# Kernel tuning notes

Hardware: AMD Instinct MI355X
Metric: run time of the kernel (lower is better)

The kernel has to match this reference:

```python
import jax, jax.numpy as jnp
import numpy as np

N_NODES = 50000
N_EDGES = 600000
N_SUB = 20000
E_SUB = 120000
D = 128

def setup_inputs() -> dict:
    key = jax.random.key(0)
    ks = jax.random.split(key, 16)
    s = 1.0 / np.sqrt(D)
    inp = {
        "x": jax.random.normal(ks[0], (N_NODES, D), dtype=jnp.float32),
        "Wm": jax.random.normal(ks[1], (D, D), dtype=jnp.float32) * s,
        "bm": jnp.zeros((D,), dtype=jnp.float32),
        "Wn2s0": jax.random.normal(ks[2], (D, D), dtype=jnp.float32) * s,
        "bn2s0": jnp.zeros((D,), dtype=jnp.float32),
        "Ws2n0": jax.random.normal(ks[3], (D, D), dtype=jnp.float32) * s,
        "bs2n0": jnp.zeros((D,), dtype=jnp.float32),
        "Wn2s1": jax.random.normal(ks[4], (D, D), dtype=jnp.float32) * s,
        "bn2s1": jnp.zeros((D,), dtype=jnp.float32),
        "Ws2n1": jax.random.normal(ks[5], (D, D), dtype=jnp.float32) * s,
        "bs2n1": jnp.zeros((D,), dtype=jnp.float32),
        "neighbor_edge_index": jax.random.randint(ks[6], (2, N_EDGES), 0, N_NODES, dtype=jnp.int64),
        "sub_row0": jax.random.randint(ks[7], (E_SUB,), 0, N_NODES, dtype=jnp.int64),
        "sub_col0": jax.random.randint(ks[8], (E_SUB,), 0, N_SUB, dtype=jnp.int64),
        "sub_row1": jax.random.randint(ks[9], (E_SUB,), 0, N_NODES, dtype=jnp.int64),
        "sub_col1": jax.random.randint(ks[10], (E_SUB,), 0, N_SUB, dtype=jnp.int64),
    }
    return inp


def _level(x, row, col, Wn2s, bn2s, Ws2n, bs2n):
    # node -> substructure: gather node feats, sum-reduce into substructures
    sub_x = jax.ops.segment_sum(x[row], col, num_segments=N_SUB)  # [n_sub, D]
    sub_x = sub_x @ Wn2s + bn2s
    # substructure -> node: gather substructure feats, sum-reduce back to nodes
    msg = jax.ops.segment_sum(sub_x[col], row, num_segments=N_NODES)  # [N, D]
    msg = msg @ Ws2n + bs2n
    return x + msg


def reference(x, Wm, bm, Wn2s0, bn2s0, Ws2n0, bs2n0, Wn2s1, bn2s1, Ws2n1, bs2n1,
              neighbor_edge_index, sub_row0, sub_col0, sub_row1, sub_col1):
    src, dst = neighbor_edge_index[0], neighbor_edge_index[1]
    # message_neighbor: GIN-like sum aggregation + Linear + ReLU
    agg = jax.ops.segment_sum(x[src], dst, num_segments=N_NODES)
    x = jax.nn.relu((x + agg) @ Wm + bm)
    # substructure levels (gather -> scatter-sum -> Linear -> gather -> scatter-sum -> Linear -> residual)
    x = _level(x, sub_row0, sub_col0, Wn2s0, bn2s0, Ws2n0, bs2n0)
    x = _level(x, sub_row1, sub_col1, Wn2s1, bn2s1, Ws2n1, bs2n1)
    return x
```

## Files before the change

kernel.cpp:

```cpp
#include <hip/hip_runtime.h>

#define D 128
#define NN 50000
#define NS 20000
#define NNP 50048
#define NSP 20032
#define L_TOT (3 * NN + 2 * NS)
#define SCAN_CHUNK 1024
#define SCAN_NBLK ((L_TOT + SCAN_CHUNK - 1) / SCAN_CHUNK)
#define LDA 136

typedef short s16x8 __attribute__((ext_vector_type(8)));
typedef float f32x4 __attribute__((ext_vector_type(4)));

__device__ __forceinline__ float b2f(unsigned int u) {
    u <<= 16;
    float f; __builtin_memcpy(&f, &u, 4);
    return f;
}
__device__ __forceinline__ unsigned short f2b(float f) {
    unsigned int u; __builtin_memcpy(&u, &f, 4);
    u += 0x7fffu + ((u >> 16) & 1u);
    return (unsigned short)(u >> 16);
}
__device__ __forceinline__ void acc8(float* a, uint4 v) {
    a[0] += b2f(v.x & 0xffffu); a[1] += b2f(v.x >> 16);
    a[2] += b2f(v.y & 0xffffu); a[3] += b2f(v.y >> 16);
    a[4] += b2f(v.z & 0xffffu); a[5] += b2f(v.z >> 16);
    a[6] += b2f(v.w & 0xffffu); a[7] += b2f(v.w >> 16);
}

struct PrepArgs {
    const float* x; unsigned short* xb;
    const float* w[5]; unsigned short* wt[5];
    int* counts;
};
#define NX4 (NN * D / 4)
#define NW  (5 * 16384)
#define NC4 (L_TOT / 4)
__global__ __launch_bounds__(256) void prep_k(PrepArgs p)
{
    int i = blockIdx.x * 256 + threadIdx.x;
    if (i < NX4) {
        float4 v = ((const float4*)p.x)[i];
        ushort4 o;
        o.x = f2b(v.x); o.y = f2b(v.y); o.z = f2b(v.z); o.w = f2b(v.w);
        ((ushort4*)p.xb)[i] = o;
        return;
    }
    i -= NX4;
    if (i < NW) {
        int wi = i >> 14;
        int r  = i & 16383;
        int k = r >> 7, n = r & 127;
        p.wt[wi][n * 128 + k] = f2b(p.w[wi][k * 128 + n]);
        return;
    }
    i -= NW;
    if (i < NC4) {
        int4 z = {0, 0, 0, 0};
        ((int4*)p.counts)[i] = z;
    }
}

__global__ __launch_bounds__(256) void hist5_k(
    const int* __restrict__ s0, const int* __restrict__ s1,
    const int* __restrict__ s2, const int* __restrict__ s3,
    const int* __restrict__ s4, int* __restrict__ counts,
    int* __restrict__ rank, int nE, int eS)
{
    int e = blockIdx.x * 256 + threadIdx.x;
    int seg, base;
    if (e < nE) { seg = s0[e]; base = 0; }
    else {
        int r = e - nE;
        if      (r <     eS) { seg = s1[r];          base = NN; }
        else if (r < 2 * eS) { seg = s2[r - eS];     base = NN + NS; }
        else if (r < 3 * eS) { seg = s3[r - 2 * eS]; base = 2 * NN + NS; }
        else if (r < 4 * eS) { seg = s4[r - 3 * eS]; base = 2 * NN + 2 * NS; }
        else return;
    }
    rank[e] = atomicAdd(&counts[base + seg], 1);
}

__global__ __launch_bounds__(256) void reduce_k(const int* __restrict__ counts,
                                                int* __restrict__ blockSums, int n)
{
    __shared__ int lds[4];
    int tid = threadIdx.x;
    int base = blockIdx.x * SCAN_CHUNK;
    int s = 0;
    #pragma unroll
    for (int i = 0; i < 4; ++i) {
        int idx = base + tid + i * 256;
        if (idx < n) s += counts[idx];
    }
    #pragma unroll
    for (int off = 32; off > 0; off >>= 1) s += __shfl_down(s, off, 64);
    if ((tid & 63) == 0) lds[tid >> 6] = s;
    __syncthreads();
    if (tid == 0) blockSums[blockIdx.x] = lds[0] + lds[1] + lds[2] + lds[3];
}

__global__ __launch_bounds__(256) void scan_sums_k(int* __restrict__ blockSums, int nb)
{
    __shared__ int lds[256];
    int tid = threadIdx.x;
    lds[tid] = (tid < nb) ? blockSums[tid] : 0;
    __syncthreads();
    for (int off = 1; off < 256; off <<= 1) {
        int t = (tid >= off) ? lds[tid - off] : 0;
        __syncthreads();
        lds[tid] += t;
        __syncthreads();
    }
    if (tid < nb) blockSums[tid] = (tid > 0) ? lds[tid - 1] : 0;
}

__global__ __launch_bounds__(256) void scan_write_k(
    const int* __restrict__ counts, const int* __restrict__ blockSums,
    int* __restrict__ offsets, int n)
{
    __shared__ int lds[256];
    int tid = threadIdx.x;
    int base = blockIdx.x * SCAN_CHUNK + tid * 4;
    int v[4]; int s = 0;
    #pragma unroll
    for (int i = 0; i < 4; ++i) {
        int idx = base + i;
        int c = (idx < n) ? counts[idx] : 0;
        v[i] = c; s += c;
    }
    lds[tid] = s;
    __syncthreads();
    for (int off = 1; off < 256; off <<= 1) {
        int t = (tid >= off) ? lds[tid - off] : 0;
        __syncthreads();
        lds[tid] += t;
        __syncthreads();
    }
    int run = blockSums[blockIdx.x] + (tid > 0 ? lds[tid - 1] : 0);
    #pragma unroll
    for (int i = 0; i < 4; ++i) {
        int idx = base + i;
        run += v[i];
        if (idx < n) offsets[idx + 1] = run;
    }
    if (blockIdx.x == 0 && tid == 0) offsets[0] = 0;
}

__global__ __launch_bounds__(256) void fill5_k(
    const int* __restrict__ s0, const int* __restrict__ v0,
    const int* __restrict__ s1, const int* __restrict__ v1,
    const int* __restrict__ s2, const int* __restrict__ v2,
    const int* __restrict__ s3, const int* __restrict__ v3,
    const int* __restrict__ s4, const int* __restrict__ v4,
    const int* __restrict__ offsets, const int* __restrict__ rank,
    int* __restrict__ perm, int nE, int eS)
{
    int e = blockIdx.x * 256 + threadIdx.x;
    int seg, val, base;
    if (e < nE) { seg = s0[e]; val = v0[e]; base = 0; }
    else {
        int r = e - nE;
        if      (r <     eS) { seg = s1[r];          val = v1[r];          base = NN; }
        else if (r < 2 * eS) { seg = s2[r - eS];     val = v2[r - eS];     base = NN + NS; }
        else if (r < 3 * eS) { seg = s3[r - 2 * eS]; val = v3[r - 2 * eS]; base = 2 * NN + NS; }
        else if (r < 4 * eS) { seg = s4[r - 3 * eS]; val = v4[r - 3 * eS]; base = 2 * NN + 2 * NS; }
        else return;
    }
    perm[offsets[base + seg] + rank[e]] = val;
}

__global__ __launch_bounds__(256, 6) void gg_k(
    const unsigned short* __restrict__ feat, const int* __restrict__ offsets,
    const int* __restrict__ perm, const unsigned short* __restrict__ addend,
    const unsigned short* __restrict__ Wt, const float* __restrict__ bias,
    const unsigned short* __restrict__ Rb, const float* __restrict__ Rf,
    float* __restrict__ outF, unsigned short* __restrict__ outB,
    int M, int relu)
{
    __shared__ unsigned short a_lds[64 * LDA];

    const int tid = threadIdx.x;
    const int r0  = blockIdx.x * 64;

    const uint4* f4 = (const uint4*)feat;
    const int lane16 = tid & 15;
    #pragma unroll
    for (int p = 0; p < 4; ++p) {
        int rloc = p * 16 + (tid >> 4);
        int s = r0 + rloc;
        float a[8] = {0.f, 0.f, 0.f, 0.f, 0.f, 0.f, 0.f, 0.f};
        if (s < M) {
            float b[8] = {0.f, 0.f, 0.f, 0.f, 0.f, 0.f, 0.f, 0.f};
            if (addend) {
                uint4 v = ((const uint4*)(addend + (size_t)s * D))[lane16];
                acc8(a, v);
            }
            int beg = offsets[s], end = offsets[s + 1];
            int j = beg;
            for (; j + 3 < end; j += 4) {
                int e0 = perm[j], e1 = perm[j + 1], e2 = perm[j + 2], e3 = perm[j + 3];
                uint4 v0 = f4[(size_t)e0 * 16 + lane16];
                uint4 v1 = f4[(size_t)e1 * 16 + lane16];
                uint4 v2 = f4[(size_t)e2 * 16 + lane16];
                uint4 v3 = f4[(size_t)e3 * 16 + lane16];
                acc8(a, v0); acc8(b, v1); acc8(a, v2); acc8(b, v3);
            }
            for (; j < end; ++j)
                acc8(a, f4[(size_t)perm[j] * 16 + lane16]);
            #pragma unroll
            for (int i = 0; i < 8; ++i) a[i] += b[i];
        }
        uint4 o;
        o.x = (unsigned int)f2b(a[0]) | ((unsigned int)f2b(a[1]) << 16);
        o.y = (unsigned int)f2b(a[2]) | ((unsigned int)f2b(a[3]) << 16);
        o.z = (unsigned int)f2b(a[4]) | ((unsigned int)f2b(a[5]) << 16);
        o.w = (unsigned int)f2b(a[6]) | ((unsigned int)f2b(a[7]) << 16);
        *((uint4*)&a_lds[rloc * LDA + lane16 * 8]) = o;
    }
    __syncthreads();

    const int lane = tid & 63;
    const int w    = tid >> 6;
    const int ln   = lane & 15;
    const int quad = lane >> 4;

    s16x8 af[4];
    const unsigned short* arow = &a_lds[(w * 16 + ln) * LDA + quad * 8];
    #pragma unroll
    for (int kc = 0; kc < 4; ++kc)
        af[kc] = *((const s16x8*)(arow + kc * 32));

    const int rbase = r0 + w * 16 + quad * 4;
    const s16x8* wt8 = (const s16x8*)Wt;

    #pragma unroll
    for (int nt = 0; nt < 8; ++nt) {
        f32x4 acc = {0.f, 0.f, 0.f, 0.f};
        const s16x8* brow = wt8 + (nt * 16 + ln) * 16 + quad;
        #pragma unroll
        for (int kc = 0; kc < 4; ++kc) {
            s16x8 bf = brow[kc * 4];
            acc = __builtin_amdgcn_mfma_f32_16x16x32_bf16(af[kc], bf, acc, 0, 0, 0);
        }
        int col = nt * 16 + ln;
        float bc = bias[col];
        #pragma unroll
        for (int r = 0; r < 4; ++r) {
            int row = rbase + r;
            if (row < M) {
                float v = acc[r] + bc;
                size_t gi = (size_t)row * D + col;
                if (Rf) v += Rf[gi];
                if (Rb) v += b2f((unsigned int)Rb[gi]);
                if (relu) v = fmaxf(v, 0.f);
                if (outF) outF[gi] = v;
                if (outB) outB[gi] = f2b(v);
            }
        }
    }
}

extern "C" void kernel_launch(void* const* d_in, const int* in_sizes, int n_in,
                              void* d_out, int out_size, void* d_ws, size_t ws_size,
                              hipStream_t stream)
{
    const float* x     = (const float*)d_in[0];
    const float* Wm    = (const float*)d_in[1];
    const float* bm    = (const float*)d_in[2];
    const float* Wn2s0 = (const float*)d_in[3];
    const float* bn2s0 = (const float*)d_in[4];
    const float* Ws2n0 = (const float*)d_in[5];
    const float* bs2n0 = (const float*)d_in[6];
    const float* Wn2s1 = (const float*)d_in[7];
    const float* bn2s1 = (const float*)d_in[8];
    const float* Ws2n1 = (const float*)d_in[9];
    const float* bs2n1 = (const float*)d_in[10];
    const int* nei  = (const int*)d_in[11];
    const int* row0 = (const int*)d_in[12];
    const int* col0 = (const int*)d_in[13];
    const int* row1 = (const int*)d_in[14];
    const int* col1 = (const int*)d_in[15];

    const int N_E = in_sizes[11] / 2;
    const int E_S = in_sizes[12];
    const int TOT_E = N_E + 4 * E_S;

    const int* src = nei;
    const int* dst = nei + N_E;

    float* out = (float*)d_out;

    unsigned short* xb   = (unsigned short*)d_ws;
    unsigned short* hbf  = xb  + (size_t)NNP * D;
    unsigned short* subb = hbf + (size_t)NNP * D;
    unsigned short* wtb  = subb + (size_t)NSP * D;
    int* ip      = (int*)(wtb + 5 * 16384);
    int* counts  = ip;              ip += L_TOT;
    int* offsets = ip;              ip += L_TOT + 1;
    int* rank    = ip;              ip += TOT_E;
    int* perm    = ip;              ip += TOT_E;
    int* bsums   = ip;              ip += 256;

    unsigned short* wt0 = wtb;
    unsigned short* wt1 = wtb + 16384;
    unsigned short* wt2 = wtb + 2 * 16384;
    unsigned short* wt3 = wtb + 3 * 16384;
    unsigned short* wt4 = wtb + 4 * 16384;

    const int* offB  = offsets;
    const int* off0c = offsets + NN;
    const int* off0r = offsets + NN + NS;
    const int* off1c = offsets + 2 * NN + NS;
    const int* off1r = offsets + 2 * NN + 2 * NS;

    dim3 blk(256);
    dim3 gTot((TOT_E + 255) / 256);
    dim3 gGemmN(NNP / 64);
    dim3 gGemmS(NSP / 64);
    dim3 gPrep((NX4 + NW + NC4 + 255) / 256);

    PrepArgs pa;
    pa.x = x; pa.xb = xb;
    pa.w[0] = Wm;  pa.w[1] = Wn2s0; pa.w[2] = Ws2n0; pa.w[3] = Wn2s1; pa.w[4] = Ws2n1;
    pa.wt[0] = wt0; pa.wt[1] = wt1; pa.wt[2] = wt2; pa.wt[3] = wt3; pa.wt[4] = wt4;
    pa.counts = counts;
    prep_k<<<gPrep, blk, 0, stream>>>(pa);

    hist5_k<<<gTot, blk, 0, stream>>>(dst, col0, row0, col1, row1, counts, rank, N_E, E_S);
    reduce_k<<<SCAN_NBLK, blk, 0, stream>>>(counts, bsums, L_TOT);
    scan_sums_k<<<1, blk, 0, stream>>>(bsums, SCAN_NBLK);
    scan_write_k<<<SCAN_NBLK, blk, 0, stream>>>(counts, bsums, offsets, L_TOT);
    fill5_k<<<gTot, blk, 0, stream>>>(dst, src, col0, row0, row0, col0,
                                      col1, row1, row1, col1, offsets, rank,
                                      perm, N_E, E_S);

    gg_k<<<gGemmN, blk, 0, stream>>>(xb, offB, perm, xb, wt0, bm,
                                     nullptr, nullptr, nullptr, hbf, NN, 1);

    gg_k<<<gGemmS, blk, 0, stream>>>(hbf, off0c, perm, nullptr, wt1, bn2s0,
                                     nullptr, nullptr, nullptr, subb, NS, 0);
    gg_k<<<gGemmN, blk, 0, stream>>>(subb, off0r, perm, nullptr, wt2, bs2n0,
                                     hbf, nullptr, out, xb, NN, 0);

    gg_k<<<gGemmS, blk, 0, stream>>>(xb, off1c, perm, nullptr, wt3, bn2s1,
                                     nullptr, nullptr, nullptr, subb, NS, 0);
    gg_k<<<gGemmN, blk, 0, stream>>>(subb, off1r, perm, nullptr, wt4, bs2n1,
                                     nullptr, out, out, nullptr, NN, 0);
}
```

Baseline: 352.8 us.

## Fuse prep with histogram, memset counts, drop fp32 residual path, raise occupancy

Merges the bf16 conversion/weight-transpose kernel and the histogram kernel into one launch, and zeroes the counts array with an async memset instead of in-kernel writes. The fp32 residual read (Rf) is removed: the level-0 output now goes only to the bf16 buffer, and the final level adds the residual from that bf16 buffer. This saves one fp32 write and one fp32 read of N×D, at the cost of rounding the residual to bf16. Launch bounds for the GEMM kernel go from 6 to 7 waves per SIMD, which can increase register pressure.

Measured after the change: 348.3 us. Within noise of the previous version (-1.3%).

```diff
diff --git a/kernel.cpp b/kernel.cpp
--- a/kernel.cpp
+++ b/kernel.cpp
@@ -30,57 +30,51 @@
     a[6] += b2f(v.w & 0xffffu); a[7] += b2f(v.w >> 16);
 }
 
-struct PrepArgs {
+#define NX4 (NN * D / 4)
+#define NW  (5 * 16384)
+#define PREP_N (NX4 + NW)
+#define PREP_BLOCKS ((PREP_N + 255) / 256)
+
+struct PrepHistArgs {
     const float* x; unsigned short* xb;
     const float* w[5]; unsigned short* wt[5];
-    int* counts;
+    const int* s0; const int* s1; const int* s2; const int* s3; const int* s4;
+    int* counts; int* rank;
+    int nE, eS;
 };
-#define NX4 (NN * D / 4)
-#define NW  (5 * 16384)
-#define NC4 (L_TOT / 4)
-__global__ __launch_bounds__(256) void prep_k(PrepArgs p)
-{
-    int i = blockIdx.x * 256 + threadIdx.x;
-    if (i < NX4) {
-        float4 v = ((const float4*)p.x)[i];
-        ushort4 o;
-        o.x = f2b(v.x); o.y = f2b(v.y); o.z = f2b(v.z); o.w = f2b(v.w);
-        ((ushort4*)p.xb)[i] = o;
+__global__ __launch_bounds__(256) void preph_k(PrepHistArgs p)
+{
+    int bid = blockIdx.x;
+    if (bid < PREP_BLOCKS) {
+        int i = bid * 256 + threadIdx.x;
+        if (i < NX4) {
+            float4 v = ((const float4*)p.x)[i];
+            ushort4 o;
+            o.x = f2b(v.x); o.y = f2b(v.y); o.z = f2b(v.z); o.w = f2b(v.w);
+            ((ushort4*)p.xb)[i] = o;
+            return;
+        }
+        i -= NX4;
+        if (i < NW) {
+            int wi = i >> 14;
+            int r  = i & 16383;
+            int k = r >> 7, n = r & 127;
+            p.wt[wi][n * 128 + k] = f2b(p.w[wi][k * 128 + n]);
+        }
         return;
     }
-    i -= NX4;
-    if (i < NW) {
-        int wi = i >> 14;
-        int r  = i & 16383;
-        int k = r >> 7, n = r & 127;
-        p.wt[wi][n * 128 + k] = f2b(p.w[wi][k * 128 + n]);
-        return;
-    }
-    i -= NW;
-    if (i < NC4) {
-        int4 z = {0, 0, 0, 0};
-        ((int4*)p.counts)[i] = z;
-    }
-}
-
-__global__ __launch_bounds__(256) void hist5_k(
-    const int* __restrict__ s0, const int* __restrict__ s1,
-    const int* __restrict__ s2, const int* __restrict__ s3,
-    const int* __restrict__ s4, int* __restrict__ counts,
-    int* __restrict__ rank, int nE, int eS)
-{
-    int e = blockIdx.x * 256 + threadIdx.x;
+    int e = (bid - PREP_BLOCKS) * 256 + threadIdx.x;
     int seg, base;
-    if (e < nE) { seg = s0[e]; base = 0; }
+    if (e < p.nE) { seg = p.s0[e]; base = 0; }
     else {
-        int r = e - nE;
-        if      (r <     eS) { seg = s1[r];          base = NN; }
-        else if (r < 2 * eS) { seg = s2[r - eS];     base = NN + NS; }
-        else if (r < 3 * eS) { seg = s3[r - 2 * eS]; base = 2 * NN + NS; }
-        else if (r < 4 * eS) { seg = s4[r - 3 * eS]; base = 2 * NN + 2 * NS; }
+        int r = e - p.nE;
+        if      (r <     p.eS) { seg = p.s1[r];            base = NN; }
+        else if (r < 2 * p.eS) { seg = p.s2[r - p.eS];     base = NN + NS; }
+        else if (r < 3 * p.eS) { seg = p.s3[r - 2 * p.eS]; base = 2 * NN + NS; }
+        else if (r < 4 * p.eS) { seg = p.s4[r - 3 * p.eS]; base = 2 * NN + 2 * NS; }
         else return;
     }
-    rank[e] = atomicAdd(&counts[base + seg], 1);
+    p.rank[e] = atomicAdd(&p.counts[base + seg], 1);
 }
 
 __global__ __launch_bounds__(256) void reduce_k(const int* __restrict__ counts,
@@ -172,11 +166,11 @@
     perm[offsets[base + seg] + rank[e]] = val;
 }
 
-__global__ __launch_bounds__(256, 6) void gg_k(
+__global__ __launch_bounds__(256, 7) void gg_k(
     const unsigned short* __restrict__ feat, const int* __restrict__ offsets,
     const int* __restrict__ perm, const unsigned short* __restrict__ addend,
     const unsigned short* __restrict__ Wt, const float* __restrict__ bias,
-    const unsigned short* __restrict__ Rb, const float* __restrict__ Rf,
+    const unsigned short* __restrict__ Rb,
     float* __restrict__ outF, unsigned short* __restrict__ outB,
     int M, int relu)
 {
@@ -253,7 +247,6 @@
             if (row < M) {
                 float v = acc[r] + bc;
                 size_t gi = (size_t)row * D + col;
-                if (Rf) v += Rf[gi];
                 if (Rb) v += b2f((unsigned int)Rb[gi]);
                 if (relu) v = fmaxf(v, 0.f);
                 if (outF) outF[gi] = v;
@@ -320,16 +313,18 @@
     dim3 gTot((TOT_E + 255) / 256);
     dim3 gGemmN(NNP / 64);
     dim3 gGemmS(NSP / 64);
-    dim3 gPrep((NX4 + NW + NC4 + 255) / 256);
-
-    PrepArgs pa;
+    dim3 gPrepH(PREP_BLOCKS + (TOT_E + 255) / 256);
+
+    hipMemsetAsync(counts, 0, L_TOT * sizeof(int), stream);
+    PrepHistArgs pa;
     pa.x = x; pa.xb = xb;
     pa.w[0] = Wm;  pa.w[1] = Wn2s0; pa.w[2] = Ws2n0; pa.w[3] = Wn2s1; pa.w[4] = Ws2n1;
     pa.wt[0] = wt0; pa.wt[1] = wt1; pa.wt[2] = wt2; pa.wt[3] = wt3; pa.wt[4] = wt4;
-    pa.counts = counts;
-    prep_k<<<gPrep, blk, 0, stream>>>(pa);
-
-    hist5_k<<<gTot, blk, 0, stream>>>(dst, col0, row0, col1, row1, counts, rank, N_E, E_S);
+    pa.s0 = dst; pa.s1 = col0; pa.s2 = row0; pa.s3 = col1; pa.s4 = row1;
+    pa.counts = counts; pa.rank = rank;
+    pa.nE = N_E; pa.eS = E_S;
+    preph_k<<<gPrepH, blk, 0, stream>>>(pa);
+
     reduce_k<<<SCAN_NBLK, blk, 0, stream>>>(counts, bsums, L_TOT);
     scan_sums_k<<<1, blk, 0, stream>>>(bsums, SCAN_NBLK);
     scan_write_k<<<SCAN_NBLK, blk, 0, stream>>>(counts, bsums, offsets, L_TOT);
@@ -338,15 +333,15 @@
                                       perm, N_E, E_S);
 
     gg_k<<<gGemmN, blk, 0, stream>>>(xb, offB, perm, xb, wt0, bm,
-                                     nullptr, nullptr, nullptr, hbf, NN, 1);
+                                     nullptr, nullptr, hbf, NN, 1);
 
     gg_k<<<gGemmS, blk, 0, stream>>>(hbf, off0c, perm, nullptr, wt1, bn2s0,
-                                     nullptr, nullptr, nullptr, subb, NS, 0);
+                                     nullptr, nullptr, subb, NS, 0);
     gg_k<<<gGemmN, blk, 0, stream>>>(subb, off0r, perm, nullptr, wt2, bs2n0,
-                                     hbf, nullptr, out, xb, NN, 0);
+                                     hbf, nullptr, xb, NN, 0);
 
     gg_k<<<gGemmS, blk, 0, stream>>>(xb, off1c, perm, nullptr, wt3, bn2s1,
-                                     nullptr, nullptr, nullptr, subb, NS, 0);
+                                     nullptr, nullptr, subb, NS, 0);
     gg_k<<<gGemmN, blk, 0, stream>>>(subb, off1r, perm, nullptr, wt4, bs2n1,
-                                     nullptr, out, out, nullptr, NN, 0);
-}
+                                     xb, out, nullptr, NN, 0);
+}
```
